# Performance work log

Hardware: AMD Instinct MI355X
Metric: run time of the kernel (lower is better)

The kernel has to match this reference:

```python
import jax, jax.numpy as jnp
import numpy as np

B, S, D, H = 2, 2048, 1024, 16
HD = D // H  # head_dim = 64


def setup_inputs() -> dict:
    key = jax.random.key(0)
    ks = jax.random.split(key, 12)
    xav = (2.0 / (D + D)) ** 0.5  # xavier_normal std for square Linear
    q = jax.random.normal(ks[0], (B, S, D), jnp.float32)
    k = jax.random.normal(ks[1], (B, S, D), jnp.float32)
    v = jax.random.normal(ks[2], (B, S, D), jnp.float32)
    Wq = jax.random.normal(ks[3], (D, D), jnp.float32) * xav
    Wk = jax.random.normal(ks[4], (D, D), jnp.float32) * xav
    Wv = jax.random.normal(ks[5], (D, D), jnp.float32) * xav
    bq = jnp.zeros((D,), jnp.float32)
    bk = jnp.zeros((D,), jnp.float32)
    bv = jnp.zeros((D,), jnp.float32)
    # valid-prefix padding masks (True = valid token); key 0 always valid so
    # no causal softmax row is fully masked (avoids NaN, matches real usage).
    klen = jax.random.randint(ks[6], (B,), S // 2, S + 1)
    qlen = jax.random.randint(ks[7], (B,), S // 2, S + 1)
    pos = jnp.arange(S)
    key_padding_mask = pos[None, :] < klen[:, None]
    query_padding_mask = pos[None, :] < qlen[:, None]
    return {
        "q": q, "k": k, "v": v,
        "Wq": Wq, "bq": bq, "Wk": Wk, "bk": bk, "Wv": Wv, "bv": bv,
        "key_padding_mask": key_padding_mask,
        "query_padding_mask": query_padding_mask,
    }


def _proj_split(x, W, b, n_heads):
    # Linear (y = x W^T + b) then split heads: [B,S,D] -> [B,H,S,hd]
    bsz, sq, dm = x.shape
    hd = dm // n_heads
    y = x @ W.T + b
    return y.reshape(bsz, sq, n_heads, hd).transpose(0, 2, 1, 3)


def reference(q, k, v, Wq, bq, Wk, bk, Wv, bv, key_padding_mask, query_padding_mask):
    bsz, sq, dm = q.shape
    sk = k.shape[1]
    Q = _proj_split(q, Wq, bq, H)  # [B,H,Sq,hd]
    K = _proj_split(k, Wk, bk, H)  # [B,H,Sk,hd]
    V = _proj_split(v, Wv, bv, H)  # [B,H,Sk,hd]
    scale = 1.0 / jnp.sqrt(jnp.asarray(Q.shape[-1], Q.dtype))
    scores = jnp.einsum('bhqd,bhkd->bhqk', Q, K) * scale  # [B,H,Sq,Sk]
    # key padding: -inf where key invalid
    scores = jnp.where(key_padding_mask[:, None, None, :], scores, -jnp.inf)
    # causal: -inf strictly above the diagonal
    causal_ok = jnp.tril(jnp.ones((sq, sk), bool))
    scores = jnp.where(causal_ok[None, None, :, :], scores, -jnp.inf)
    attn = jax.nn.softmax(scores, axis=-1)
    # q_mask: zero out rows for padded queries (post-softmax, as in source)
    attn = jnp.where(query_padding_mask[:, None, :, None], attn, 0.0)
    # dropout p=0.0 -> identity
    out = jnp.einsum('bhqk,bhkd->bhqd', attn, V)
    out = out.transpose(0, 2, 1, 3).reshape(bsz, sq, dm)
    return out + q
```

## Files before the change

### kernel.cpp

```cpp
#include <hip/hip_runtime.h>
#include <stdint.h>

#define BATCH 2
#define SEQ 2048
#define DMODEL 1024
#define NHEAD 16
#define HDIM 64
#define CVT_BLOCKS 15360

typedef __attribute__((ext_vector_type(8))) short bf16x8;
typedef __attribute__((ext_vector_type(4))) float f32x4;

__device__ __forceinline__ unsigned short f2bf(float f) {
  unsigned int u = __float_as_uint(f);
  u += 0x7fffu + ((u >> 16) & 1u);
  return (unsigned short)(u >> 16);
}
__device__ __forceinline__ unsigned int pk2bf(float a, float b) {
  return __builtin_amdgcn_perm(__float_as_uint(b) + 0x8000u,
                               __float_as_uint(a) + 0x8000u, 0x07060302u);
}
__device__ __forceinline__ void async_copy16(const void* g, void* l) {
  __builtin_amdgcn_global_load_lds(
      (const __attribute__((address_space(1))) void*)g,
      (__attribute__((address_space(3))) void*)l, 16, 0, 0);
}

__global__ __launch_bounds__(256) void cvt_all(
    const float* __restrict__ q, const float* __restrict__ k,
    const float* __restrict__ v, const float* __restrict__ Wq,
    const float* __restrict__ Wk, const float* __restrict__ Wv,
    unsigned short* __restrict__ dst,
    const unsigned char* __restrict__ kp, const unsigned char* __restrict__ qp,
    int* __restrict__ lens) {
  if (blockIdx.x == CVT_BLOCKS) {
    const int t = threadIdx.x, wave = t >> 6, lane = t & 63;
    const unsigned char* base = (wave < 2) ? kp : qp;
    const int b = wave & 1;
    const bool bytefmt = (base[1] != 0);
    int cnt = 0;
    if (bytefmt) {
      const uint4* p = (const uint4*)(base + (size_t)b * SEQ);
#pragma unroll
      for (int g = 0; g < 2; g++) {
        const uint4 x = p[g * 64 + lane];
        const unsigned int w[4] = {x.x, x.y, x.z, x.w};
#pragma unroll
        for (int i = 0; i < 4; i++) {
          const unsigned int ww = w[i];
          cnt += ((ww & 0xffu) != 0) + ((ww & 0xff00u) != 0) +
                 ((ww & 0xff0000u) != 0) + ((ww & 0xff000000u) != 0);
        }
      }
    } else {
      const uint4* p = (const uint4*)(base + (size_t)b * SEQ * 4);
#pragma unroll
      for (int g = 0; g < 8; g++) {
        const uint4 x = p[g * 64 + lane];
        cnt += (x.x != 0) + (x.y != 0) + (x.z != 0) + (x.w != 0);
      }
    }
#pragma unroll
    for (int off = 32; off >= 1; off >>= 1) cnt += __shfl_xor(cnt, off, 64);
    if (lane == 0) lens[wave] = cnt;
    return;
  }
  const int g = blockIdx.x * 256 + threadIdx.x;
  const float* src;
  size_t off, dbase;
  if (g < 3 * (1 << 20)) {
    const int ti = g >> 20;
    src = (ti == 0) ? q : (ti == 1) ? k : v;
    off = (size_t)(g & ((1 << 20) - 1));
    dbase = (size_t)ti << 22;
  } else {
    const int gw = g - 3 * (1 << 20);
    const int ti = gw >> 18;
    src = (ti == 0) ? Wq : (ti == 1) ? Wk : Wv;
    off = (size_t)(gw & ((1 << 18) - 1));
    dbase = (3ull << 22) + ((size_t)ti << 20);
  }
  const float4 x = ((const float4*)src)[off];
  ushort4 o;
  o.x = f2bf(x.x); o.y = f2bf(x.y); o.z = f2bf(x.z); o.w = f2bf(x.w);
  *(ushort4*)(dst + dbase + off * 4) = o;
}

__global__ __launch_bounds__(256) void qkv_proj(
    const unsigned short* __restrict__ xq, const unsigned short* __restrict__ xk,
    const unsigned short* __restrict__ xv,
    const unsigned short* __restrict__ Wq, const float* __restrict__ bq,
    const unsigned short* __restrict__ Wk, const float* __restrict__ bk,
    const unsigned short* __restrict__ Wv, const float* __restrict__ bv,
    unsigned short* __restrict__ Qo, unsigned short* __restrict__ Ko,
    unsigned short* __restrict__ Vo) {
  const int z = blockIdx.z;
  const unsigned short* x = (z == 0) ? xq : (z == 1) ? xk : xv;
  const unsigned short* W = (z == 0) ? Wq : (z == 1) ? Wk : Wv;
  const float* bias = (z == 0) ? bq : (z == 1) ? bk : bv;
  unsigned short* dst = (z == 0) ? Qo : (z == 1) ? Ko : Vo;
  const float osc = (z == 0) ? 0.18033688011112042f : 1.0f;

  __shared__ unsigned short As[128 * 32];
  __shared__ unsigned short Bs[128 * 32];

  const int t = threadIdx.x;
  const int wave = t >> 6, lane = t & 63, quad = lane >> 4, l16 = lane & 15;
  const int wm = wave >> 1, wn = wave & 1;
  const int m0 = blockIdx.y * 128, n0 = blockIdx.x * 128;

  const f32x4 fz = {0.f, 0.f, 0.f, 0.f};
  f32x4 acc[4][4];
#pragma unroll
  for (int i = 0; i < 4; i++)
#pragma unroll
    for (int j = 0; j < 4; j++) acc[i][j] = fz;

  for (int k0 = 0; k0 < DMODEL; k0 += 32) {
    __syncthreads();
#pragma unroll
    for (int c = 0; c < 2; c++) {
      const int g = c * 256 + t;
      const int row = g >> 2, cc = g & 3;
      async_copy16(x + (size_t)(m0 + row) * DMODEL + k0 + cc * 8,
                   (char*)As + (c * 256 + (t & 192)) * 16);
      async_copy16(W + (size_t)(n0 + row) * DMODEL + k0 + cc * 8,
                   (char*)Bs + (c * 256 + (t & 192)) * 16);
    }
    __syncthreads();
    bf16x8 af[4], bfr[4];
#pragma unroll
    for (int i = 0; i < 4; i++) {
      af[i] = *(const bf16x8*)(As + (wm * 64 + i * 16 + l16) * 32 + quad * 8);
      bfr[i] = *(const bf16x8*)(Bs + (wn * 64 + i * 16 + l16) * 32 + quad * 8);
    }
#pragma unroll
    for (int i = 0; i < 4; i++)
#pragma unroll
      for (int j = 0; j < 4; j++)
        acc[i][j] = __builtin_amdgcn_mfma_f32_16x16x32_bf16(af[i], bfr[j], acc[i][j], 0, 0, 0);
  }

#pragma unroll
  for (int j = 0; j < 4; j++) {
    const int n = n0 + wn * 64 + j * 16 + l16;
    const float bf_ = bias[n];
    const int h = n >> 6, hd = n & 63;
#pragma unroll
    for (int i = 0; i < 4; i++) {
#pragma unroll
      for (int r = 0; r < 4; r++) {
        const int m = m0 + wm * 64 + i * 16 + quad * 4 + r;
        const int bb = m >> 11, s = m & (SEQ - 1);
        dst[(((size_t)(bb * NHEAD + h) * SEQ + s) << 6) + hd] = f2bf((acc[i][j][r] + bf_) * osc);
      }
    }
  }
}


template <bool MASKED>
__device__ __forceinline__ void softmax_update(
    const f32x4 s[8], int key0, int qrow, int klen, int quad, int l16,
    float& mst, float& lsum, f32x4 o[4], unsigned short* Pdst) {
  float pm[8][4];
  float rm = -__builtin_inff();
  if (MASKED) {
    const int kmax = ((qrow < klen - 1) ? qrow : klen - 1) - key0 - quad * 4;
#pragma unroll
    for (int nf = 0; nf < 8; nf++)
#pragma unroll
      for (int r = 0; r < 4; r++) {
        pm[nf][r] = (nf * 16 + r <= kmax) ? s[nf][r] : -__builtin_inff();
        rm = fmaxf(rm, pm[nf][r]);
      }
  } else {
#pragma unroll
    for (int nf = 0; nf < 8; nf++)
#pragma unroll
      for (int r = 0; r < 4; r++) {
        pm[nf][r] = s[nf][r];
        rm = fmaxf(rm, pm[nf][r]);
      }
  }
  rm = fmaxf(rm, __shfl_xor(rm, 16, 64));
  rm = fmaxf(rm, __shfl_xor(rm, 32, 64));
  if (__ballot(rm > mst) != 0ull) {
    const float mnew = fmaxf(mst, rm);
    const float alpha = exp2f(fmaxf(mst, -1e30f) - fmaxf(mnew, -1e30f));
    mst = mnew;
    lsum *= alpha;
    float ab[4];
#pragma unroll
    for (int r = 0; r < 4; r++) ab[r] = __shfl(alpha, quad * 4 + r, 64);
#pragma unroll
    for (int db = 0; db < 4; db++)
#pragma unroll
      for (int r = 0; r < 4; r++) o[db][r] *= ab[r];
  }
  const float mref = fmaxf(mst, -1e30f);
  float rs = 0.f;
#pragma unroll
  for (int nf = 0; nf < 8; nf++)
#pragma unroll
    for (int r = 0; r < 4; r++) {
      const float p = exp2f(pm[nf][r] - mref);
      pm[nf][r] = p;
      rs += p;
    }
  rs += __shfl_xor(rs, 16, 64);
  rs += __shfl_xor(rs, 32, 64);
  lsum += rs;
#pragma unroll
  for (int nf = 0; nf < 8; nf++) {
    uint2 w;
    w.x = pk2bf(pm[nf][0], pm[nf][1]);
    w.y = pk2bf(pm[nf][2], pm[nf][3]);
    const int grp = (nf * 2 + (quad >> 1)) ^ l16;
    *(uint2*)(Pdst + l16 * 128 + grp * 8 + (quad & 1) * 4) = w;
  }
}

__global__ __launch_bounds__(256, 2) void attn_kernel(
    const unsigned short* __restrict__ Qb, const unsigned short* __restrict__ Kb,
    const unsigned short* __restrict__ Vb, const float* __restrict__ qin,
    const int* __restrict__ lens, float* __restrict__ out) {
  const int qi = 31 - blockIdx.x, h = blockIdx.y, b = blockIdx.z;
  const int bh = b * NHEAD + h;
  const int t = threadIdx.x, wave = t >> 6, lane = t & 63, quad = lane >> 4, l16 = lane & 15;
  const int klen = lens[b], qlen = lens[2 + b];

  if (qi * 64 >= qlen) {
    const int row = qi * 64 + (t >> 2);
    const size_t base = (size_t)(b * SEQ + row) * DMODEL + h * HDIM;
    const float4* src = (const float4*)(qin + base);
    float4* dst = (float4*)(out + base);
#pragma unroll
    for (int c = 0; c < 4; c++) dst[(t & 3) * 4 + c] = src[(t & 3) * 4 + c];
    return;
  }

  __shared__ unsigned short Ks[128 * 64];
  __shared__ unsigned short VT[64 * 128];
  __shared__ unsigned short Ps[4][16 * 128];

  const unsigned short* Qp = Qb + (size_t)bh * SEQ * HDIM;
  const unsigned short* Kp = Kb + (size_t)bh * SEQ * HDIM;
  const unsigned short* Vp = Vb + (size_t)bh * SEQ * HDIM;

  const int qrow = qi * 64 + wave * 16 + l16;
  const bf16x8 qf0 = *(const bf16x8*)(Qp + (size_t)qrow * HDIM + quad * 8);
  const bf16x8 qf1 = *(const bf16x8*)(Qp + (size_t)qrow * HDIM + 32 + quad * 8);

  const f32x4 fz = {0.f, 0.f, 0.f, 0.f};
  f32x4 o[4];
#pragma unroll
  for (int i = 0; i < 4; i++) o[i] = fz;
  float mst = -__builtin_inff(), lsum = 0.f;

  const int kend = ((qi * 64 + 64) < klen) ? (qi * 64 + 64) : klen;
  const int ktot = (kend + 127) >> 7;

  for (int kt = 0; kt < ktot; kt++) {
    const int key0 = kt << 7;
    __syncthreads();
#pragma unroll
    for (int c = 0; c < 4; c++) {
      const int slot = c * 256 + t;
      const int row = slot >> 3, pg = slot & 7;
      async_copy16(Kp + (size_t)(key0 + row) * HDIM + (pg ^ (row & 7)) * 8,
                   (char*)Ks + (c * 256 + (t & 192)) * 16);
    }
#pragma unroll
    for (int c = 0; c < 4; c++) {
      const int slot = c * 256 + t;
      const int key = slot >> 3, u = slot & 7, d8 = u * 8;
      const bf16x8 vv = *(const bf16x8*)(Vp + (size_t)(key0 + key) * HDIM + d8);
      const int K16 = key >> 3, k7 = key & 7;
#pragma unroll
      for (int jj = 0; jj < 8; jj++) {
        const int j = (jj + u) & 7;
        const int d = d8 + j;
        VT[d * 128 + ((K16 ^ (d & 15)) * 8) + k7] = ((const unsigned short*)&vv)[j];
      }
    }
    __syncthreads();

    f32x4 s[8];
#pragma unroll
    for (int nf = 0; nf < 8; nf++) {
      const int row = nf * 16 + l16;
      const int sw = row & 7;
      const bf16x8 kf0 = *(const bf16x8*)(Ks + row * 64 + (quad ^ sw) * 8);
      const bf16x8 kf1 = *(const bf16x8*)(Ks + row * 64 + ((quad + 4) ^ sw) * 8);
      f32x4 a = fz;
      a = __builtin_amdgcn_mfma_f32_16x16x32_bf16(kf0, qf0, a, 0, 0, 0);
      a = __builtin_amdgcn_mfma_f32_16x16x32_bf16(kf1, qf1, a, 0, 0, 0);
      s[nf] = a;
    }

    const bool nomask = (key0 + 127 <= qi * 64) && (key0 + 127 < klen);
    if (nomask)
      softmax_update<false>(s, key0, qrow, klen, quad, l16, mst, lsum, o, Ps[wave]);
    else
      softmax_update<true>(s, key0, qrow, klen, quad, l16, mst, lsum, o, Ps[wave]);

    bf16x8 pf[4];
#pragma unroll
    for (int ks = 0; ks < 4; ks++)
      pf[ks] = *(const bf16x8*)(Ps[wave] + l16 * 128 + ((ks * 4 + quad) ^ l16) * 8);
#pragma unroll
    for (int db = 0; db < 4; db++) {
      const int d = db * 16 + l16;
#pragma unroll
      for (int ks = 0; ks < 4; ks++) {
        const bf16x8 vt = *(const bf16x8*)(VT + d * 128 + ((ks * 4 + quad) ^ l16) * 8);
        o[db] = __builtin_amdgcn_mfma_f32_16x16x32_bf16(pf[ks], vt, o[db], 0, 0, 0);
      }
    }
  }

  const float invv = (lsum > 0.f) ? 1.f / lsum : 0.f;
  float ib[4];
#pragma unroll
  for (int r = 0; r < 4; r++) ib[r] = __shfl(invv, quad * 4 + r, 64);
#pragma unroll
  for (int db = 0; db < 4; db++) {
    const int col = h * HDIM + db * 16 + l16;
#pragma unroll
    for (int r = 0; r < 4; r++) {
      const int i = qi * 64 + wave * 16 + quad * 4 + r;
      const size_t idx = (size_t)(b * SEQ + i) * DMODEL + col;
      out[idx] = ((i < qlen) ? o[db][r] * ib[r] : 0.f) + qin[idx];
    }
  }
}

extern "C" void kernel_launch(void* const* d_in, const int* in_sizes, int n_in,
                              void* d_out, int out_size, void* d_ws, size_t ws_size,
                              hipStream_t stream) {
  (void)in_sizes; (void)n_in; (void)out_size; (void)ws_size;
  const float* q = (const float*)d_in[0];
  const float* k = (const float*)d_in[1];
  const float* v = (const float*)d_in[2];
  const float* Wq = (const float*)d_in[3];
  const float* bq = (const float*)d_in[4];
  const float* Wk = (const float*)d_in[5];
  const float* bk = (const float*)d_in[6];
  const float* Wv = (const float*)d_in[7];
  const float* bv = (const float*)d_in[8];
  const unsigned char* kpm = (const unsigned char*)d_in[9];
  const unsigned char* qpm = (const unsigned char*)d_in[10];
  float* out = (float*)d_out;

  const size_t tsz = (size_t)BATCH * SEQ * DMODEL;
  const size_t wsz = (size_t)DMODEL * DMODEL;

  char* ws = (char*)d_ws;
  int* lens = (int*)ws;
  unsigned short* cvt_base = (unsigned short*)(ws + 256);
  unsigned short* qb16 = cvt_base;
  unsigned short* kb16 = qb16 + tsz;
  unsigned short* vb16 = kb16 + tsz;
  unsigned short* Wqb = vb16 + tsz;
  unsigned short* Wkb = Wqb + wsz;
  unsigned short* Wvb = Wkb + wsz;
  unsigned short* Qw = Wvb + wsz;
  unsigned short* Kw = Qw + tsz;
  unsigned short* Vw = Kw + tsz;

  cvt_all<<<dim3(CVT_BLOCKS + 1), dim3(256), 0, stream>>>(q, k, v, Wq, Wk, Wv,
                                                          cvt_base, kpm, qpm, lens);
  qkv_proj<<<dim3(8, 32, 3), dim3(256), 0, stream>>>(qb16, kb16, vb16, Wqb, bq, Wkb, bk, Wvb, bv, Qw, Kw, Vw);
  attn_kernel<<<dim3(32, NHEAD, BATCH), dim3(256), 0, stream>>>(Qw, Kw, Vw, q, lens, out);
}
```

Measured before the change: 251.0 us.

## Emit transposed V from projection and pair causal query tiles per block

The QKV projection now writes V already transposed per head, using swapped MFMA operands so the output is head-dim-major. The attention kernel can then fill its V tile with async global-to-LDS copies instead of scalar transposing stores. Each attention block now handles a low and a high query tile (lo, 31-lo), which balances causal work across blocks and shares each K/V tile load between the two. Occupancy is raised to 3 blocks per SM in the launch bounds. The cost is more register pressure from the two sets of accumulators, and the transposed V stores in the projection are strided.

```diff
diff --git a/kernel.cpp b/kernel.cpp
--- a/kernel.cpp
+++ b/kernel.cpp
@@ -134,25 +134,51 @@
       af[i] = *(const bf16x8*)(As + (wm * 64 + i * 16 + l16) * 32 + quad * 8);
       bfr[i] = *(const bf16x8*)(Bs + (wn * 64 + i * 16 + l16) * 32 + quad * 8);
     }
-#pragma unroll
-    for (int i = 0; i < 4; i++)
-#pragma unroll
-      for (int j = 0; j < 4; j++)
-        acc[i][j] = __builtin_amdgcn_mfma_f32_16x16x32_bf16(af[i], bfr[j], acc[i][j], 0, 0, 0);
-  }
-
-#pragma unroll
-  for (int j = 0; j < 4; j++) {
-    const int n = n0 + wn * 64 + j * 16 + l16;
-    const float bf_ = bias[n];
-    const int h = n >> 6, hd = n & 63;
-#pragma unroll
-    for (int i = 0; i < 4; i++) {
-#pragma unroll
-      for (int r = 0; r < 4; r++) {
-        const int m = m0 + wm * 64 + i * 16 + quad * 4 + r;
-        const int bb = m >> 11, s = m & (SEQ - 1);
-        dst[(((size_t)(bb * NHEAD + h) * SEQ + s) << 6) + hd] = f2bf((acc[i][j][r] + bf_) * osc);
+    if (z == 2) {
+#pragma unroll
+      for (int i = 0; i < 4; i++)
+#pragma unroll
+        for (int j = 0; j < 4; j++)
+          acc[i][j] = __builtin_amdgcn_mfma_f32_16x16x32_bf16(bfr[j], af[i], acc[i][j], 0, 0, 0);
+    } else {
+#pragma unroll
+      for (int i = 0; i < 4; i++)
+#pragma unroll
+        for (int j = 0; j < 4; j++)
+          acc[i][j] = __builtin_amdgcn_mfma_f32_16x16x32_bf16(af[i], bfr[j], acc[i][j], 0, 0, 0);
+    }
+  }
+
+  if (z == 2) {
+#pragma unroll
+    for (int j = 0; j < 4; j++) {
+#pragma unroll
+      for (int i = 0; i < 4; i++) {
+#pragma unroll
+        for (int r = 0; r < 4; r++) {
+          const int n = n0 + wn * 64 + j * 16 + quad * 4 + r;
+          const int m = m0 + wm * 64 + i * 16 + l16;
+          const int bb = m >> 11, s = m & (SEQ - 1);
+          const int hh = n >> 6, hd = n & 63;
+          dst[(((size_t)(bb * NHEAD + hh) * HDIM + hd) << 11) + s] =
+              f2bf(acc[i][j][r] + bias[n]);
+        }
+      }
+    }
+  } else {
+#pragma unroll
+    for (int j = 0; j < 4; j++) {
+      const int n = n0 + wn * 64 + j * 16 + l16;
+      const float bf_ = bias[n];
+      const int hh = n >> 6, hd = n & 63;
+#pragma unroll
+      for (int i = 0; i < 4; i++) {
+#pragma unroll
+        for (int r = 0; r < 4; r++) {
+          const int m = m0 + wm * 64 + i * 16 + quad * 4 + r;
+          const int bb = m >> 11, s = m & (SEQ - 1);
+          dst[(((size_t)(bb * NHEAD + hh) * SEQ + s) << 6) + hd] = f2bf((acc[i][j][r] + bf_) * osc);
+        }
       }
     }
   }
@@ -221,24 +247,33 @@
   }
 }
 
-__global__ __launch_bounds__(256, 2) void attn_kernel(
+__device__ __forceinline__ void pv_accum(f32x4 o[4], const unsigned short* Pw,
+                                         const unsigned short* vt, int quad, int l16) {
+  bf16x8 pf[4];
+#pragma unroll
+  for (int ks = 0; ks < 4; ks++)
+    pf[ks] = *(const bf16x8*)(Pw + l16 * 128 + ((ks * 4 + quad) ^ l16) * 8);
+#pragma unroll
+  for (int db = 0; db < 4; db++) {
+    const int d = db * 16 + l16;
+#pragma unroll
+    for (int ks = 0; ks < 4; ks++) {
+      const bf16x8 v = *(const bf16x8*)(vt + d * 128 + ((ks * 4 + quad) ^ l16) * 8);
+      o[db] = __builtin_amdgcn_mfma_f32_16x16x32_bf16(pf[ks], v, o[db], 0, 0, 0);
+    }
+  }
+}
+
+__global__ __launch_bounds__(256, 3) void attn_kernel(
     const unsigned short* __restrict__ Qb, const unsigned short* __restrict__ Kb,
-    const unsigned short* __restrict__ Vb, const float* __restrict__ qin,
+    const unsigned short* __restrict__ VTb, const float* __restrict__ qin,
     const int* __restrict__ lens, float* __restrict__ out) {
-  const int qi = 31 - blockIdx.x, h = blockIdx.y, b = blockIdx.z;
+  const int pi = blockIdx.x, h = blockIdx.y, b = blockIdx.z;
+  const int lo = pi, hi = 31 - pi;
   const int bh = b * NHEAD + h;
   const int t = threadIdx.x, wave = t >> 6, lane = t & 63, quad = lane >> 4, l16 = lane & 15;
   const int klen = lens[b], qlen = lens[2 + b];
-
-  if (qi * 64 >= qlen) {
-    const int row = qi * 64 + (t >> 2);
-    const size_t base = (size_t)(b * SEQ + row) * DMODEL + h * HDIM;
-    const float4* src = (const float4*)(qin + base);
-    float4* dst = (float4*)(out + base);
-#pragma unroll
-    for (int c = 0; c < 4; c++) dst[(t & 3) * 4 + c] = src[(t & 3) * 4 + c];
-    return;
-  }
+  const bool doHI = (hi * 64 < qlen);
 
   __shared__ unsigned short Ks[128 * 64];
   __shared__ unsigned short VT[64 * 128];
@@ -246,20 +281,30 @@
 
   const unsigned short* Qp = Qb + (size_t)bh * SEQ * HDIM;
   const unsigned short* Kp = Kb + (size_t)bh * SEQ * HDIM;
-  const unsigned short* Vp = Vb + (size_t)bh * SEQ * HDIM;
-
-  const int qrow = qi * 64 + wave * 16 + l16;
-  const bf16x8 qf0 = *(const bf16x8*)(Qp + (size_t)qrow * HDIM + quad * 8);
-  const bf16x8 qf1 = *(const bf16x8*)(Qp + (size_t)qrow * HDIM + 32 + quad * 8);
+  const unsigned short* Vt = VTb + (size_t)bh * HDIM * SEQ;
+
+  const int qrLO = lo * 64 + wave * 16 + l16;
+  const int qrHI = hi * 64 + wave * 16 + l16;
+  const bf16x8 qlo0 = *(const bf16x8*)(Qp + (size_t)qrLO * HDIM + quad * 8);
+  const bf16x8 qlo1 = *(const bf16x8*)(Qp + (size_t)qrLO * HDIM + 32 + quad * 8);
+  const bf16x8 qhi0 = *(const bf16x8*)(Qp + (size_t)qrHI * HDIM + quad * 8);
+  const bf16x8 qhi1 = *(const bf16x8*)(Qp + (size_t)qrHI * HDIM + 32 + quad * 8);
 
   const f32x4 fz = {0.f, 0.f, 0.f, 0.f};
-  f32x4 o[4];
-#pragma unroll
-  for (int i = 0; i < 4; i++) o[i] = fz;
-  float mst = -__builtin_inff(), lsum = 0.f;
-
-  const int kend = ((qi * 64 + 64) < klen) ? (qi * 64 + 64) : klen;
-  const int ktot = (kend + 127) >> 7;
+  f32x4 oLO[4], oHI[4];
+#pragma unroll
+  for (int i = 0; i < 4; i++) { oLO[i] = fz; oHI[i] = fz; }
+  float mLO = -__builtin_inff(), lLO = 0.f;
+  float mHI = -__builtin_inff(), lHI = 0.f;
+
+  const int kendLO = ((lo * 64 + 64) < klen) ? (lo * 64 + 64) : klen;
+  const int ktotLO = (kendLO + 127) >> 7;
+  int ktotHI = 0;
+  if (doHI) {
+    const int kendHI = ((hi * 64 + 64) < klen) ? (hi * 64 + 64) : klen;
+    ktotHI = (kendHI + 127) >> 7;
+  }
+  const int ktot = (ktotHI > ktotLO) ? ktotHI : ktotLO;
 
   for (int kt = 0; kt < ktot; kt++) {
     const int key0 = kt << 7;
@@ -274,64 +319,68 @@
 #pragma unroll
     for (int c = 0; c < 4; c++) {
       const int slot = c * 256 + t;
-      const int key = slot >> 3, u = slot & 7, d8 = u * 8;
-      const bf16x8 vv = *(const bf16x8*)(Vp + (size_t)(key0 + key) * HDIM + d8);
-      const int K16 = key >> 3, k7 = key & 7;
-#pragma unroll
-      for (int jj = 0; jj < 8; jj++) {
-        const int j = (jj + u) & 7;
-        const int d = d8 + j;
-        VT[d * 128 + ((K16 ^ (d & 15)) * 8) + k7] = ((const unsigned short*)&vv)[j];
-      }
+      const int row = slot >> 4, pg = slot & 15;
+      async_copy16(Vt + (size_t)row * SEQ + key0 + (pg ^ (row & 15)) * 8,
+                   (char*)VT + (c * 256 + (t & 192)) * 16);
     }
     __syncthreads();
 
-    f32x4 s[8];
+    const bool cLO = (kt < ktotLO), cHI = (kt < ktotHI);
+    f32x4 sLO[8], sHI[8];
 #pragma unroll
     for (int nf = 0; nf < 8; nf++) {
       const int row = nf * 16 + l16;
       const int sw = row & 7;
       const bf16x8 kf0 = *(const bf16x8*)(Ks + row * 64 + (quad ^ sw) * 8);
       const bf16x8 kf1 = *(const bf16x8*)(Ks + row * 64 + ((quad + 4) ^ sw) * 8);
-      f32x4 a = fz;
-      a = __builtin_amdgcn_mfma_f32_16x16x32_bf16(kf0, qf0, a, 0, 0, 0);
-      a = __builtin_amdgcn_mfma_f32_16x16x32_bf16(kf1, qf1, a, 0, 0, 0);
-      s[nf] = a;
-    }
-
-    const bool nomask = (key0 + 127 <= qi * 64) && (key0 + 127 < klen);
-    if (nomask)
-      softmax_update<false>(s, key0, qrow, klen, quad, l16, mst, lsum, o, Ps[wave]);
-    else
-      softmax_update<true>(s, key0, qrow, klen, quad, l16, mst, lsum, o, Ps[wave]);
-
-    bf16x8 pf[4];
-#pragma unroll
-    for (int ks = 0; ks < 4; ks++)
-      pf[ks] = *(const bf16x8*)(Ps[wave] + l16 * 128 + ((ks * 4 + quad) ^ l16) * 8);
-#pragma unroll
-    for (int db = 0; db < 4; db++) {
-      const int d = db * 16 + l16;
-#pragma unroll
-      for (int ks = 0; ks < 4; ks++) {
-        const bf16x8 vt = *(const bf16x8*)(VT + d * 128 + ((ks * 4 + quad) ^ l16) * 8);
-        o[db] = __builtin_amdgcn_mfma_f32_16x16x32_bf16(pf[ks], vt, o[db], 0, 0, 0);
-      }
-    }
-  }
-
-  const float invv = (lsum > 0.f) ? 1.f / lsum : 0.f;
-  float ib[4];
-#pragma unroll
-  for (int r = 0; r < 4; r++) ib[r] = __shfl(invv, quad * 4 + r, 64);
+      if (cHI) {
+        f32x4 a = fz;
+        a = __builtin_amdgcn_mfma_f32_16x16x32_bf16(kf0, qhi0, a, 0, 0, 0);
+        a = __builtin_amdgcn_mfma_f32_16x16x32_bf16(kf1, qhi1, a, 0, 0, 0);
+        sHI[nf] = a;
+      }
+      if (cLO) {
+        f32x4 a = fz;
+        a = __builtin_amdgcn_mfma_f32_16x16x32_bf16(kf0, qlo0, a, 0, 0, 0);
+        a = __builtin_amdgcn_mfma_f32_16x16x32_bf16(kf1, qlo1, a, 0, 0, 0);
+        sLO[nf] = a;
+      }
+    }
+    if (cHI) {
+      if ((key0 + 127 <= hi * 64) && (key0 + 127 < klen))
+        softmax_update<false>(sHI, key0, qrHI, klen, quad, l16, mHI, lHI, oHI, Ps[wave]);
+      else
+        softmax_update<true>(sHI, key0, qrHI, klen, quad, l16, mHI, lHI, oHI, Ps[wave]);
+      pv_accum(oHI, Ps[wave], VT, quad, l16);
+    }
+    if (cLO) {
+      if ((key0 + 127 <= lo * 64) && (key0 + 127 < klen))
+        softmax_update<false>(sLO, key0, qrLO, klen, quad, l16, mLO, lLO, oLO, Ps[wave]);
+      else
+        softmax_update<true>(sLO, key0, qrLO, klen, quad, l16, mLO, lLO, oLO, Ps[wave]);
+      pv_accum(oLO, Ps[wave], VT, quad, l16);
+    }
+  }
+
+  const float invLO = (lLO > 0.f) ? 1.f / lLO : 0.f;
+  const float invHI = (lHI > 0.f) ? 1.f / lHI : 0.f;
+  float ibLO[4], ibHI[4];
+#pragma unroll
+  for (int r = 0; r < 4; r++) {
+    ibLO[r] = __shfl(invLO, quad * 4 + r, 64);
+    ibHI[r] = __shfl(invHI, quad * 4 + r, 64);
+  }
 #pragma unroll
   for (int db = 0; db < 4; db++) {
     const int col = h * HDIM + db * 16 + l16;
 #pragma unroll
     for (int r = 0; r < 4; r++) {
-      const int i = qi * 64 + wave * 16 + quad * 4 + r;
-      const size_t idx = (size_t)(b * SEQ + i) * DMODEL + col;
-      out[idx] = ((i < qlen) ? o[db][r] * ib[r] : 0.f) + qin[idx];
+      const int iL = lo * 64 + wave * 16 + quad * 4 + r;
+      const int iH = hi * 64 + wave * 16 + quad * 4 + r;
+      const size_t oL = (size_t)(b * SEQ + iL) * DMODEL + col;
+      const size_t oH = (size_t)(b * SEQ + iH) * DMODEL + col;
+      out[oL] = ((iL < qlen) ? oLO[db][r] * ibLO[r] : 0.f) + qin[oL];
+      out[oH] = ((iH < qlen) ? oHI[db][r] * ibHI[r] : 0.f) + qin[oH];
     }
   }
 }
@@ -367,10 +416,10 @@
   unsigned short* Wvb = Wkb + wsz;
   unsigned short* Qw = Wvb + wsz;
   unsigned short* Kw = Qw + tsz;
-  unsigned short* Vw = Kw + tsz;
+  unsigned short* Vtw = Kw + tsz;
 
   cvt_all<<<dim3(CVT_BLOCKS + 1), dim3(256), 0, stream>>>(q, k, v, Wq, Wk, Wv,
                                                           cvt_base, kpm, qpm, lens);
-  qkv_proj<<<dim3(8, 32, 3), dim3(256), 0, stream>>>(qb16, kb16, vb16, Wqb, bq, Wkb, bk, Wvb, bv, Qw, Kw, Vw);
-  attn_kernel<<<dim3(32, NHEAD, BATCH), dim3(256), 0, stream>>>(Qw, Kw, Vw, q, lens, out);
-}
+  qkv_proj<<<dim3(8, 32, 3), dim3(256), 0, stream>>>(qb16, kb16, vb16, Wqb, bq, Wkb, bk, Wvb, bv, Qw, Kw, Vtw);
+  attn_kernel<<<dim3(16, NHEAD, BATCH), dim3(256), 0, stream>>>(Qw, Kw, Vtw, q, lens, out);
+}
```

After: 297.6 us. 1.19x slower.
